# Optimization experiments

Measured on AMD Instinct MI355X. Metric: run time of the kernel, lower is better.

Reference implementation:

```python
import jax, jax.numpy as jnp
import numpy as np

B, NQ, NK = 8, 16384, 16384
FEAT, MID, CTX, OUT = 128, 16, 128, 128
EPS = 1e-5


def setup_inputs() -> dict:
    key = jax.random.key(0)
    ks = jax.random.split(key, 7)
    s_in = 1.0 / np.sqrt(FEAT)
    s_ctx = 1.0 / np.sqrt(CTX)
    return {
        "feature": jax.random.normal(ks[0], (B, NQ, FEAT), dtype=jnp.float32),
        "context": jax.random.normal(ks[1], (B, NK, CTX), dtype=jnp.float32),
        "Wq": jax.random.uniform(ks[2], (FEAT, MID), jnp.float32, -s_in, s_in),
        "Wk": jax.random.uniform(ks[3], (CTX, MID), jnp.float32, -s_ctx, s_ctx),
        "Wv": jax.random.uniform(ks[4], (CTX, OUT), jnp.float32, -s_ctx, s_ctx),
        "gamma": jnp.ones((MID,), jnp.float32),
        "beta": jnp.zeros((MID,), jnp.float32),
    }


def reference(feature, context, Wq, Wk, Wv, gamma, beta):
    # per-token linear projections (QKVTransformV2 with heads=1)
    query = feature @ Wq                     # [B, Nq, mid]
    key = context @ Wk                       # [B, Nk, mid]
    value = context @ Wv                     # [B, Nk, out]
    # softmax over context positions (dim=1)
    sm = jax.nn.softmax(key, axis=1)         # [B, Nk, mid]
    # content lambda: softmax^T @ value -> [B, mid, out]
    lam = jnp.einsum("bnm,bnd->bmd", sm, value)
    # BatchNorm1d(mid) in training mode: stats over (batch, length=out)
    mean = jnp.mean(lam, axis=(0, 2), keepdims=True)
    var = jnp.var(lam, axis=(0, 2), keepdims=True)  # biased, matches torch BN
    bn = (lam - mean) * jax.lax.rsqrt(var + EPS)
    bn = bn * gamma[None, :, None] + beta[None, :, None]
    # final query matmul -> [B, Nq, out]
    return jnp.einsum("bqm,bmd->bqd", query, bn)
```

## Files before the change

kernel.cpp:

```cpp
#include <hip/hip_runtime.h>
#include <cstddef>

#define BATCH 8
#define NQ 16384
#define NK 16384
#define FEAT 128
#define MID 16
#define CTXD 128
#define OUTD 128
#define EPSV 1e-5f

#define OFF_LAM 0
#define OFF_ST  16384
#define OFF_SW  16448
#define OFF_U   16576
#define OFF_S   32960
#define OFF_P   49408
#define NEED_FLOATS (49408 + 8 * 128 * 16 * 128)

__device__ __forceinline__ float readlane_f(float v, int lane) {
    return __uint_as_float(__builtin_amdgcn_readlane(__float_as_uint(v), lane));
}

template <bool PARTIALS>
__global__ __launch_bounds__(256) void k_phase1(
    const float* __restrict__ ctx, const float* __restrict__ Wk,
    float* __restrict__ P, float* __restrict__ S,
    float* __restrict__ U, float* __restrict__ sumwG)
{
    __shared__ float cL[64 * 132];
    __shared__ float wkL[128 * 16];
    const int b    = blockIdx.y;
    const int blk  = blockIdx.x;
    const int t    = threadIdx.x;
    const int lane = t & 63;
    const int g    = __builtin_amdgcn_readfirstlane(t >> 6);

    #pragma unroll
    for (int i = 0; i < 8; ++i) wkL[t + 256 * i] = Wk[t + 256 * i];

    float a00 = 0.f, a01 = 0.f, a10 = 0.f, a11 = 0.f;
    float a20 = 0.f, a21 = 0.f, a30 = 0.f, a31 = 0.f;
    float sw0 = 0.f, sw1 = 0.f, sw2 = 0.f, sw3 = 0.f;
    const size_t rowbase = (size_t)b * NK + (size_t)blk * 128;

    for (int s = 0; s < 2; ++s) {
        __syncthreads();
        {
            const float4* g4 = (const float4*)(ctx + (rowbase + 64 * s) * CTXD);
            float4* c4p = (float4*)cL;
            #pragma unroll
            for (int i = 0; i < 8; ++i) {
                int idx = t + 256 * i;
                c4p[(idx >> 5) * 33 + (idx & 31)] = g4[idx];
            }
        }
        __syncthreads();

        float k0 = 0.f, k1 = 0.f, k2 = 0.f, k3 = 0.f;
        {
            const float4* cr = (const float4*)cL + lane * 33;
            #pragma unroll 8
            for (int kq = 0; kq < 32; ++kq) {
                float4 c4  = cr[kq];
                float4 wr0 = *(const float4*)(wkL + (4 * kq + 0) * 16 + 4 * g);
                float4 wr1 = *(const float4*)(wkL + (4 * kq + 1) * 16 + 4 * g);
                float4 wr2 = *(const float4*)(wkL + (4 * kq + 2) * 16 + 4 * g);
                float4 wr3 = *(const float4*)(wkL + (4 * kq + 3) * 16 + 4 * g);
                k0 += c4.x * wr0.x + c4.y * wr1.x + c4.z * wr2.x + c4.w * wr3.x;
                k1 += c4.x * wr0.y + c4.y * wr1.y + c4.z * wr2.y + c4.w * wr3.y;
                k2 += c4.x * wr0.z + c4.y * wr1.z + c4.z * wr2.z + c4.w * wr3.z;
                k3 += c4.x * wr0.w + c4.y * wr1.w + c4.z * wr2.w + c4.w * wr3.w;
            }
        }
        float w0 = __expf(k0), w1 = __expf(k1), w2 = __expf(k2), w3 = __expf(k3);

        {
            float s0 = w0, s1 = w1, s2 = w2, s3 = w3;
            #pragma unroll
            for (int off = 32; off > 0; off >>= 1) {
                s0 += __shfl_xor(s0, off); s1 += __shfl_xor(s1, off);
                s2 += __shfl_xor(s2, off); s3 += __shfl_xor(s3, off);
            }
            sw0 += s0; sw1 += s1; sw2 += s2; sw3 += s3;
        }

        #pragma unroll 4
        for (int n = 0; n < 64; ++n) {
            float b0 = readlane_f(w0, n);
            float b1 = readlane_f(w1, n);
            float b2 = readlane_f(w2, n);
            float b3 = readlane_f(w3, n);
            float2 c2 = *(const float2*)(cL + n * 132 + 2 * lane);
            a00 += b0 * c2.x; a01 += b0 * c2.y;
            a10 += b1 * c2.x; a11 += b1 * c2.y;
            a20 += b2 * c2.x; a21 += b2 * c2.y;
            a30 += b3 * c2.x; a31 += b3 * c2.y;
        }
    }

    if (PARTIALS) {
        float2* p0 = (float2*)(P + (((size_t)b * 128 + blk) * 16 + 4 * g) * 128 + 2 * lane);
        p0[0]          = make_float2(a00, a01);
        p0[64]         = make_float2(a10, a11);
        p0[128]        = make_float2(a20, a21);
        p0[192]        = make_float2(a30, a31);
        if (lane == 0) {
            S[((size_t)b * 16 + 4 * g + 0) * 128 + blk] = sw0;
            S[((size_t)b * 16 + 4 * g + 1) * 128 + blk] = sw1;
            S[((size_t)b * 16 + 4 * g + 2) * 128 + blk] = sw2;
            S[((size_t)b * 16 + 4 * g + 3) * 128 + blk] = sw3;
        }
    } else {
        float* u0 = U + ((size_t)b * 16 + 4 * g) * 128 + 2 * lane;
        atomicAdd(u0 + 0,   a00); atomicAdd(u0 + 1,   a01);
        atomicAdd(u0 + 128, a10); atomicAdd(u0 + 129, a11);
        atomicAdd(u0 + 256, a20); atomicAdd(u0 + 257, a21);
        atomicAdd(u0 + 384, a30); atomicAdd(u0 + 385, a31);
        if (lane == 0) {
            atomicAdd(&sumwG[b * 16 + 4 * g + 0], sw0);
            atomicAdd(&sumwG[b * 16 + 4 * g + 1], sw1);
            atomicAdd(&sumwG[b * 16 + 4 * g + 2], sw2);
            atomicAdd(&sumwG[b * 16 + 4 * g + 3], sw3);
        }
    }
}

template <bool PARTIALS>
__global__ __launch_bounds__(256) void k_lam(
    const float* __restrict__ P, const float* __restrict__ S,
    const float* __restrict__ U, const float* __restrict__ sumwG,
    const float* __restrict__ Wv, float* __restrict__ lam, float* __restrict__ st)
{
    const int m = blockIdx.x, b = blockIdx.y, t = threadIdx.x;
    __shared__ float uL[128];
    __shared__ float red[256];
    __shared__ float swL;
    const int d = t & 127, h = t >> 7;

    float acc = 0.f;
    if (PARTIALS) {
        const float* p = P + ((size_t)b * 128 * 16 + m) * 128 + d;
        for (int blk = h; blk < 128; blk += 2) acc += p[(size_t)blk * 2048];
    } else {
        if (h == 0) acc = U[((size_t)b * 16 + m) * 128 + d];
    }
    red[t] = acc;

    if (t < 64) {
        float s;
        if (PARTIALS) {
            const float* sp = S + ((size_t)b * 16 + m) * 128;
            s = sp[t] + sp[t + 64];
            #pragma unroll
            for (int off = 32; off > 0; off >>= 1) s += __shfl_xor(s, off);
        } else {
            s = sumwG[b * 16 + m];
        }
        if (t == 0) swL = s;
    }
    __syncthreads();
    if (t < 128) uL[t] = red[t] + red[t + 128];
    __syncthreads();

    float dot = 0.f;
    const float* wv = Wv + h * 64 * OUTD + d;
    #pragma unroll 8
    for (int k = 0; k < 64; ++k) dot += uL[h * 64 + k] * wv[k * OUTD];
    red[t] = dot;
    __syncthreads();
    if (t < 128) {
        float l = (red[t] + red[t + 128]) / swL;
        lam[((size_t)b * 16 + m) * 128 + t] = l;
        float s1 = l, s2 = l * l;
        #pragma unroll
        for (int off = 32; off > 0; off >>= 1) {
            s1 += __shfl_xor(s1, off);
            s2 += __shfl_xor(s2, off);
        }
        if ((t & 63) == 0) {
            atomicAdd(&st[m], s1);
            atomicAdd(&st[16 + m], s2);
        }
    }
}

__global__ __launch_bounds__(256) void k_out(
    const float* __restrict__ feat, const float* __restrict__ Wq,
    const float* __restrict__ lam, const float* __restrict__ st,
    const float* __restrict__ gamma, const float* __restrict__ beta,
    float* __restrict__ out)
{
    __shared__ float fL[64 * 132];
    __shared__ float bnL[16 * 132];
    __shared__ float wqL[128 * 16];
    const int b    = blockIdx.y;
    const int t    = threadIdx.x;
    const int lane = t & 63;
    const size_t r0 = (size_t)blockIdx.x * 64;

    #pragma unroll
    for (int i = 0; i < 8; ++i) wqL[t + 256 * i] = Wq[t + 256 * i];

    #pragma unroll
    for (int i = 0; i < 8; ++i) {
        int e = t + 256 * i;
        int m = e >> 7, d = e & 127;
        float mean = st[m] * (1.f / (BATCH * OUTD));
        float var  = st[16 + m] * (1.f / (BATCH * OUTD)) - mean * mean;
        bnL[m * 132 + d] =
            (lam[((size_t)b * 16 + m) * 128 + d] - mean) * rsqrtf(var + EPSV) * gamma[m] + beta[m];
    }
    {
        const float4* g4 = (const float4*)(feat + ((size_t)b * NQ + r0) * FEAT);
        float4* f4p = (float4*)fL;
        #pragma unroll
        for (int i = 0; i < 8; ++i) {
            int idx = t + 256 * i;
            f4p[(idx >> 5) * 33 + (idx & 31)] = g4[idx];
        }
    }
    __syncthreads();

    float q0 = 0.f, q1 = 0.f, q2 = 0.f, q3 = 0.f;
    {
        const int g = __builtin_amdgcn_readfirstlane(t >> 6);
        const float4* fr = (const float4*)fL + lane * 33;
        #pragma unroll 8
        for (int kq = 0; kq < 32; ++kq) {
            float4 c4  = fr[kq];
            float4 wr0 = *(const float4*)(wqL + (4 * kq + 0) * 16 + 4 * g);
            float4 wr1 = *(const float4*)(wqL + (4 * kq + 1) * 16 + 4 * g);
            float4 wr2 = *(const float4*)(wqL + (4 * kq + 2) * 16 + 4 * g);
            float4 wr3 = *(const float4*)(wqL + (4 * kq + 3) * 16 + 4 * g);
            q0 += c4.x * wr0.x + c4.y * wr1.x + c4.z * wr2.x + c4.w * wr3.x;
            q1 += c4.x * wr0.y + c4.y * wr1.y + c4.z * wr2.y + c4.w * wr3.y;
            q2 += c4.x * wr0.z + c4.y * wr1.z + c4.z * wr2.z + c4.w * wr3.z;
            q3 += c4.x * wr0.w + c4.y * wr1.w + c4.z * wr2.w + c4.w * wr3.w;
        }
    }
    __syncthreads();
    {
        const int g = __builtin_amdgcn_readfirstlane(t >> 6);
        ((float4*)fL)[lane * 5 + g] = make_float4(q0, q1, q2, q3);
    }
    __syncthreads();

    {
        const int nblk = t >> 4;
        const int dq   = t & 15;
        const float4* qL4  = (const float4*)fL;
        const float4* bnL4 = (const float4*)bnL;
        float qv[4][16];
        #pragma unroll
        for (int rr = 0; rr < 4; ++rr) {
            #pragma unroll
            for (int mq = 0; mq < 4; ++mq) {
                float4 v = qL4[(4 * nblk + rr) * 5 + mq];
                qv[rr][4 * mq + 0] = v.x; qv[rr][4 * mq + 1] = v.y;
                qv[rr][4 * mq + 2] = v.z; qv[rr][4 * mq + 3] = v.w;
            }
        }
        float accv[4][8];
        #pragma unroll
        for (int rr = 0; rr < 4; ++rr)
            #pragma unroll
            for (int j = 0; j < 8; ++j) accv[rr][j] = 0.f;

        #pragma unroll
        for (int m = 0; m < 16; ++m) {
            float4 b0 = bnL4[m * 33 + 2 * dq];
            float4 b1 = bnL4[m * 33 + 2 * dq + 1];
            #pragma unroll
            for (int rr = 0; rr < 4; ++rr) {
                float qq = qv[rr][m];
                accv[rr][0] += qq * b0.x; accv[rr][1] += qq * b0.y;
                accv[rr][2] += qq * b0.z; accv[rr][3] += qq * b0.w;
                accv[rr][4] += qq * b1.x; accv[rr][5] += qq * b1.y;
                accv[rr][6] += qq * b1.z; accv[rr][7] += qq * b1.w;
            }
        }
        #pragma unroll
        for (int rr = 0; rr < 4; ++rr) {
            float4* op = (float4*)(out + ((size_t)b * NQ + r0 + 4 * nblk + rr) * OUTD + 8 * dq);
            op[0] = make_float4(accv[rr][0], accv[rr][1], accv[rr][2], accv[rr][3]);
            op[1] = make_float4(accv[rr][4], accv[rr][5], accv[rr][6], accv[rr][7]);
        }
    }
}

extern "C" void kernel_launch(void* const* d_in, const int* in_sizes, int n_in,
                              void* d_out, int out_size, void* d_ws, size_t ws_size,
                              hipStream_t stream)
{
    const float* feat  = (const float*)d_in[0];
    const float* ctx   = (const float*)d_in[1];
    const float* Wq    = (const float*)d_in[2];
    const float* Wk    = (const float*)d_in[3];
    const float* Wv    = (const float*)d_in[4];
    const float* gamma = (const float*)d_in[5];
    const float* beta  = (const float*)d_in[6];
    float* out = (float*)d_out;

    float* ws    = (float*)d_ws;
    float* lam   = ws + OFF_LAM;
    float* st    = ws + OFF_ST;
    float* sumwG = ws + OFF_SW;
    float* U     = ws + OFF_U;
    float* S     = ws + OFF_S;
    float* P     = ws + OFF_P;

    const bool partials = ws_size >= (size_t)NEED_FLOATS * sizeof(float);

    if (partials) {
        hipMemsetAsync((char*)d_ws + OFF_ST * sizeof(float), 0, 64 * sizeof(float), stream);
        k_phase1<true><<<dim3(128, BATCH), 256, 0, stream>>>(ctx, Wk, P, S, U, sumwG);
        k_lam<true><<<dim3(MID, BATCH), 256, 0, stream>>>(P, S, U, sumwG, Wv, lam, st);
    } else {
        hipMemsetAsync((char*)d_ws + OFF_ST * sizeof(float), 0,
                       (OFF_U + 16384 - OFF_ST) * sizeof(float), stream);
        k_phase1<false><<<dim3(128, BATCH), 256, 0, stream>>>(ctx, Wk, P, S, U, sumwG);
        k_lam<false><<<dim3(MID, BATCH), 256, 0, stream>>>(P, S, U, sumwG, Wv, lam, st);
    }
    k_out<<<dim3(NQ / 64, BATCH), 256, 0, stream>>>(feat, Wq, lam, st, gamma, beta, out);
}
```

Baseline: 222.3 us.

## Fold Wq into BN lambda and use bf16 MFMA for key and output matmuls

Precomputes E = Wq @ bn(lambda) per batch as a bf16 128x128 matrix in a new small kernel, so the output kernel becomes one feature @ E matmul done with bf16 MFMA instead of two fp32 FMA stages. The key projection in phase1 also moves to bf16 MFMA, with swizzled LDS layouts and an LDS-staged exp-weight buffer in place of readlane broadcasts. This cuts ALU work in both memory-heavy kernels and adds one extra tiny launch. Rounding inputs to bf16 lowers precision, which affects the softmax exponent and the output.

```diff
diff --git a/kernel.cpp b/kernel.cpp
--- a/kernel.cpp
+++ b/kernel.cpp
@@ -14,12 +14,24 @@
 #define OFF_ST  16384
 #define OFF_SW  16448
 #define OFF_U   16576
-#define OFF_S   32960
-#define OFF_P   49408
-#define NEED_FLOATS (49408 + 8 * 128 * 16 * 128)
-
-__device__ __forceinline__ float readlane_f(float v, int lane) {
-    return __uint_as_float(__builtin_amdgcn_readlane(__float_as_uint(v), lane));
+#define OFF_E   32960
+#define OFF_S   98496
+#define OFF_P   114880
+#define NEED_FLOATS (114880 + 2097152)
+
+typedef __attribute__((ext_vector_type(8))) short bf16x8;
+typedef __attribute__((ext_vector_type(4))) float f32x4;
+
+__device__ __forceinline__ short f2bf(float x) {
+    union { float f; unsigned u; } v; v.f = x;
+    unsigned r = v.u + 0x7fffu + ((v.u >> 16) & 1u);
+    return (short)(r >> 16);
+}
+__device__ __forceinline__ bf16x8 pack8(float4 a, float4 b) {
+    bf16x8 r;
+    r[0] = f2bf(a.x); r[1] = f2bf(a.y); r[2] = f2bf(a.z); r[3] = f2bf(a.w);
+    r[4] = f2bf(b.x); r[5] = f2bf(b.y); r[6] = f2bf(b.z); r[7] = f2bf(b.w);
+    return r;
 }
 
 template <bool PARTIALS>
@@ -28,101 +40,93 @@
     float* __restrict__ P, float* __restrict__ S,
     float* __restrict__ U, float* __restrict__ sumwG)
 {
-    __shared__ float cL[64 * 132];
-    __shared__ float wkL[128 * 16];
-    const int b    = blockIdx.y;
-    const int blk  = blockIdx.x;
-    const int t    = threadIdx.x;
+    __shared__ float cL[64 * 128];
+    __shared__ short wkT[16 * 136];
+    __shared__ float wL[64 * 20];
+    __shared__ float swred[4][16];
+    const int b = blockIdx.y, blk = blockIdx.x, t = threadIdx.x;
     const int lane = t & 63;
-    const int g    = __builtin_amdgcn_readfirstlane(t >> 6);
-
-    #pragma unroll
-    for (int i = 0; i < 8; ++i) wkL[t + 256 * i] = Wk[t + 256 * i];
-
-    float a00 = 0.f, a01 = 0.f, a10 = 0.f, a11 = 0.f;
-    float a20 = 0.f, a21 = 0.f, a30 = 0.f, a31 = 0.f;
-    float sw0 = 0.f, sw1 = 0.f, sw2 = 0.f, sw3 = 0.f;
+    const int wid  = __builtin_amdgcn_readfirstlane(t >> 6);
+    const int rlo = lane & 15, h = lane >> 4;
+
+    #pragma unroll
+    for (int i = 0; i < 8; ++i) {
+        int e = t + 256 * i;
+        wkT[(e & 15) * 136 + (e >> 4)] = f2bf(Wk[e]);
+    }
+
+    float a00=0.f,a01=0.f,a10=0.f,a11=0.f,a20=0.f,a21=0.f,a30=0.f,a31=0.f;
+    float sw = 0.f;
     const size_t rowbase = (size_t)b * NK + (size_t)blk * 128;
 
     for (int s = 0; s < 2; ++s) {
         __syncthreads();
         {
             const float4* g4 = (const float4*)(ctx + (rowbase + 64 * s) * CTXD);
-            float4* c4p = (float4*)cL;
             #pragma unroll
             for (int i = 0; i < 8; ++i) {
                 int idx = t + 256 * i;
-                c4p[(idx >> 5) * 33 + (idx & 31)] = g4[idx];
+                int r = idx >> 5, c = idx & 31;
+                ((float4*)cL)[r * 32 + (c ^ (r & 7))] = g4[idx];
             }
         }
         __syncthreads();
 
-        float k0 = 0.f, k1 = 0.f, k2 = 0.f, k3 = 0.f;
-        {
-            const float4* cr = (const float4*)cL + lane * 33;
-            #pragma unroll 8
-            for (int kq = 0; kq < 32; ++kq) {
-                float4 c4  = cr[kq];
-                float4 wr0 = *(const float4*)(wkL + (4 * kq + 0) * 16 + 4 * g);
-                float4 wr1 = *(const float4*)(wkL + (4 * kq + 1) * 16 + 4 * g);
-                float4 wr2 = *(const float4*)(wkL + (4 * kq + 2) * 16 + 4 * g);
-                float4 wr3 = *(const float4*)(wkL + (4 * kq + 3) * 16 + 4 * g);
-                k0 += c4.x * wr0.x + c4.y * wr1.x + c4.z * wr2.x + c4.w * wr3.x;
-                k1 += c4.x * wr0.y + c4.y * wr1.y + c4.z * wr2.y + c4.w * wr3.y;
-                k2 += c4.x * wr0.z + c4.y * wr1.z + c4.z * wr2.z + c4.w * wr3.z;
-                k3 += c4.x * wr0.w + c4.y * wr1.w + c4.z * wr2.w + c4.w * wr3.w;
-            }
-        }
-        float w0 = __expf(k0), w1 = __expf(k1), w2 = __expf(k2), w3 = __expf(k3);
-
-        {
-            float s0 = w0, s1 = w1, s2 = w2, s3 = w3;
-            #pragma unroll
-            for (int off = 32; off > 0; off >>= 1) {
-                s0 += __shfl_xor(s0, off); s1 += __shfl_xor(s1, off);
-                s2 += __shfl_xor(s2, off); s3 += __shfl_xor(s3, off);
-            }
-            sw0 += s0; sw1 += s1; sw2 += s2; sw3 += s3;
-        }
-
-        #pragma unroll 4
+        const int row = wid * 16 + rlo;
+        f32x4 kacc = {0.f, 0.f, 0.f, 0.f};
+        #pragma unroll
+        for (int ks = 0; ks < 4; ++ks) {
+            float4 A0 = ((const float4*)cL)[row * 32 + ((8*ks + 2*h)     ^ (row & 7))];
+            float4 A1 = ((const float4*)cL)[row * 32 + ((8*ks + 2*h + 1) ^ (row & 7))];
+            bf16x8 af = pack8(A0, A1);
+            bf16x8 bq = *(const bf16x8*)(wkT + rlo * 136 + 32*ks + 8*h);
+            kacc = __builtin_amdgcn_mfma_f32_16x16x32_bf16(af, bq, kacc, 0, 0, 0);
+        }
+        float w0 = __expf(kacc[0]);
+        float w1 = __expf(kacc[1]);
+        float w2 = __expf(kacc[2]);
+        float w3 = __expf(kacc[3]);
+        sw += w0 + w1 + w2 + w3;
+        const int nb = wid * 16 + 4 * h;
+        wL[(nb + 0) * 20 + rlo] = w0;
+        wL[(nb + 1) * 20 + rlo] = w1;
+        wL[(nb + 2) * 20 + rlo] = w2;
+        wL[(nb + 3) * 20 + rlo] = w3;
+        __syncthreads();
+
+        #pragma unroll 8
         for (int n = 0; n < 64; ++n) {
-            float b0 = readlane_f(w0, n);
-            float b1 = readlane_f(w1, n);
-            float b2 = readlane_f(w2, n);
-            float b3 = readlane_f(w3, n);
-            float2 c2 = *(const float2*)(cL + n * 132 + 2 * lane);
-            a00 += b0 * c2.x; a01 += b0 * c2.y;
-            a10 += b1 * c2.x; a11 += b1 * c2.y;
-            a20 += b2 * c2.x; a21 += b2 * c2.y;
-            a30 += b3 * c2.x; a31 += b3 * c2.y;
+            float4 w4 = *(const float4*)(wL + n * 20 + 4 * wid);
+            const float2 c2 = *(const float2*)((const char*)cL + n * 512
+                               + ((((lane >> 1) ^ (n & 7))) << 4) + ((lane & 1) << 3));
+            a00 += w4.x * c2.x; a01 += w4.x * c2.y;
+            a10 += w4.y * c2.x; a11 += w4.y * c2.y;
+            a20 += w4.z * c2.x; a21 += w4.z * c2.y;
+            a30 += w4.w * c2.x; a31 += w4.w * c2.y;
         }
     }
 
     if (PARTIALS) {
-        float2* p0 = (float2*)(P + (((size_t)b * 128 + blk) * 16 + 4 * g) * 128 + 2 * lane);
-        p0[0]          = make_float2(a00, a01);
-        p0[64]         = make_float2(a10, a11);
-        p0[128]        = make_float2(a20, a21);
-        p0[192]        = make_float2(a30, a31);
-        if (lane == 0) {
-            S[((size_t)b * 16 + 4 * g + 0) * 128 + blk] = sw0;
-            S[((size_t)b * 16 + 4 * g + 1) * 128 + blk] = sw1;
-            S[((size_t)b * 16 + 4 * g + 2) * 128 + blk] = sw2;
-            S[((size_t)b * 16 + 4 * g + 3) * 128 + blk] = sw3;
-        }
+        float2* p0 = (float2*)(P + (((size_t)b * 128 + blk) * 16 + 4 * wid) * 128 + 2 * lane);
+        p0[0]   = make_float2(a00, a01);
+        p0[64]  = make_float2(a10, a11);
+        p0[128] = make_float2(a20, a21);
+        p0[192] = make_float2(a30, a31);
     } else {
-        float* u0 = U + ((size_t)b * 16 + 4 * g) * 128 + 2 * lane;
+        float* u0 = U + ((size_t)b * 16 + 4 * wid) * 128 + 2 * lane;
         atomicAdd(u0 + 0,   a00); atomicAdd(u0 + 1,   a01);
         atomicAdd(u0 + 128, a10); atomicAdd(u0 + 129, a11);
         atomicAdd(u0 + 256, a20); atomicAdd(u0 + 257, a21);
         atomicAdd(u0 + 384, a30); atomicAdd(u0 + 385, a31);
-        if (lane == 0) {
-            atomicAdd(&sumwG[b * 16 + 4 * g + 0], sw0);
-            atomicAdd(&sumwG[b * 16 + 4 * g + 1], sw1);
-            atomicAdd(&sumwG[b * 16 + 4 * g + 2], sw2);
-            atomicAdd(&sumwG[b * 16 + 4 * g + 3], sw3);
-        }
+    }
+    sw += __shfl_xor(sw, 16);
+    sw += __shfl_xor(sw, 32);
+    if (lane < 16) swred[wid][lane] = sw;
+    __syncthreads();
+    if (t < 16) {
+        float tot = swred[0][t] + swred[1][t] + swred[2][t] + swred[3][t];
+        if (PARTIALS) S[((size_t)b * 16 + t) * 128 + blk] = tot;
+        else          atomicAdd(&sumwG[b * 16 + t], tot);
     }
 }
 
@@ -185,107 +189,91 @@
     }
 }
 
-__global__ __launch_bounds__(256) void k_out(
-    const float* __restrict__ feat, const float* __restrict__ Wq,
+__global__ __launch_bounds__(256) void k_E(
     const float* __restrict__ lam, const float* __restrict__ st,
-    const float* __restrict__ gamma, const float* __restrict__ beta,
-    float* __restrict__ out)
-{
-    __shared__ float fL[64 * 132];
-    __shared__ float bnL[16 * 132];
-    __shared__ float wqL[128 * 16];
-    const int b    = blockIdx.y;
-    const int t    = threadIdx.x;
-    const int lane = t & 63;
-    const size_t r0 = (size_t)blockIdx.x * 64;
-
-    #pragma unroll
-    for (int i = 0; i < 8; ++i) wqL[t + 256 * i] = Wq[t + 256 * i];
-
+    const float* __restrict__ Wq, const float* __restrict__ gamma,
+    const float* __restrict__ beta, short* __restrict__ Ebuf)
+{
+    const int b = blockIdx.x, t = threadIdx.x;
+    __shared__ float bnL[16 * 128];
+    __shared__ float wqL[128 * 20];
+    #pragma unroll
+    for (int i = 0; i < 8; ++i) {
+        int e = t + 256 * i;
+        wqL[(e >> 4) * 20 + (e & 15)] = Wq[e];
+    }
     #pragma unroll
     for (int i = 0; i < 8; ++i) {
         int e = t + 256 * i;
         int m = e >> 7, d = e & 127;
         float mean = st[m] * (1.f / (BATCH * OUTD));
         float var  = st[16 + m] * (1.f / (BATCH * OUTD)) - mean * mean;
-        bnL[m * 132 + d] =
-            (lam[((size_t)b * 16 + m) * 128 + d] - mean) * rsqrtf(var + EPSV) * gamma[m] + beta[m];
-    }
+        bnL[m * 128 + d] = (lam[((size_t)b * 16 + m) * 128 + d] - mean)
+                           * rsqrtf(var + EPSV) * gamma[m] + beta[m];
+    }
+    __syncthreads();
+    const int k = t & 127, dh = t >> 7;
+    float wq[16];
+    #pragma unroll
+    for (int j = 0; j < 4; ++j) {
+        float4 v = ((const float4*)wqL)[k * 5 + j];
+        wq[4*j] = v.x; wq[4*j+1] = v.y; wq[4*j+2] = v.z; wq[4*j+3] = v.w;
+    }
+    short* eb = Ebuf + (size_t)b * 16384;
+    #pragma unroll 4
+    for (int i = 0; i < 64; ++i) {
+        int d = dh + 2 * i;
+        float s = 0.f;
+        #pragma unroll
+        for (int m = 0; m < 16; ++m) s += wq[m] * bnL[m * 128 + d];
+        eb[d * 128 + k] = f2bf(s);
+    }
+}
+
+__global__ __launch_bounds__(256) void k_out(
+    const float* __restrict__ feat, const short* __restrict__ Ebuf,
+    float* __restrict__ out)
+{
+    __shared__ short eL[128 * 128];
+    const int b = blockIdx.y, t = threadIdx.x;
+    const int lane = t & 63;
+    const int wid  = __builtin_amdgcn_readfirstlane(t >> 6);
+    const int rlo = lane & 15, h = lane >> 4;
+    const size_t r0 = (size_t)blockIdx.x * 64;
+
     {
-        const float4* g4 = (const float4*)(feat + ((size_t)b * NQ + r0) * FEAT);
-        float4* f4p = (float4*)fL;
+        const float4* esrc = (const float4*)(Ebuf + (size_t)b * 16384);
         #pragma unroll
         for (int i = 0; i < 8; ++i) {
             int idx = t + 256 * i;
-            f4p[(idx >> 5) * 33 + (idx & 31)] = g4[idx];
-        }
-    }
-    __syncthreads();
-
-    float q0 = 0.f, q1 = 0.f, q2 = 0.f, q3 = 0.f;
-    {
-        const int g = __builtin_amdgcn_readfirstlane(t >> 6);
-        const float4* fr = (const float4*)fL + lane * 33;
-        #pragma unroll 8
-        for (int kq = 0; kq < 32; ++kq) {
-            float4 c4  = fr[kq];
-            float4 wr0 = *(const float4*)(wqL + (4 * kq + 0) * 16 + 4 * g);
-            float4 wr1 = *(const float4*)(wqL + (4 * kq + 1) * 16 + 4 * g);
-            float4 wr2 = *(const float4*)(wqL + (4 * kq + 2) * 16 + 4 * g);
-            float4 wr3 = *(const float4*)(wqL + (4 * kq + 3) * 16 + 4 * g);
-            q0 += c4.x * wr0.x + c4.y * wr1.x + c4.z * wr2.x + c4.w * wr3.x;
-            q1 += c4.x * wr0.y + c4.y * wr1.y + c4.z * wr2.y + c4.w * wr3.y;
-            q2 += c4.x * wr0.z + c4.y * wr1.z + c4.z * wr2.z + c4.w * wr3.z;
-            q3 += c4.x * wr0.w + c4.y * wr1.w + c4.z * wr2.w + c4.w * wr3.w;
-        }
-    }
-    __syncthreads();
-    {
-        const int g = __builtin_amdgcn_readfirstlane(t >> 6);
-        ((float4*)fL)[lane * 5 + g] = make_float4(q0, q1, q2, q3);
-    }
-    __syncthreads();
-
-    {
-        const int nblk = t >> 4;
-        const int dq   = t & 15;
-        const float4* qL4  = (const float4*)fL;
-        const float4* bnL4 = (const float4*)bnL;
-        float qv[4][16];
-        #pragma unroll
-        for (int rr = 0; rr < 4; ++rr) {
-            #pragma unroll
-            for (int mq = 0; mq < 4; ++mq) {
-                float4 v = qL4[(4 * nblk + rr) * 5 + mq];
-                qv[rr][4 * mq + 0] = v.x; qv[rr][4 * mq + 1] = v.y;
-                qv[rr][4 * mq + 2] = v.z; qv[rr][4 * mq + 3] = v.w;
-            }
-        }
-        float accv[4][8];
-        #pragma unroll
-        for (int rr = 0; rr < 4; ++rr)
-            #pragma unroll
-            for (int j = 0; j < 8; ++j) accv[rr][j] = 0.f;
-
-        #pragma unroll
-        for (int m = 0; m < 16; ++m) {
-            float4 b0 = bnL4[m * 33 + 2 * dq];
-            float4 b1 = bnL4[m * 33 + 2 * dq + 1];
-            #pragma unroll
-            for (int rr = 0; rr < 4; ++rr) {
-                float qq = qv[rr][m];
-                accv[rr][0] += qq * b0.x; accv[rr][1] += qq * b0.y;
-                accv[rr][2] += qq * b0.z; accv[rr][3] += qq * b0.w;
-                accv[rr][4] += qq * b1.x; accv[rr][5] += qq * b1.y;
-                accv[rr][6] += qq * b1.z; accv[rr][7] += qq * b1.w;
-            }
-        }
-        #pragma unroll
-        for (int rr = 0; rr < 4; ++rr) {
-            float4* op = (float4*)(out + ((size_t)b * NQ + r0 + 4 * nblk + rr) * OUTD + 8 * dq);
-            op[0] = make_float4(accv[rr][0], accv[rr][1], accv[rr][2], accv[rr][3]);
-            op[1] = make_float4(accv[rr][4], accv[rr][5], accv[rr][6], accv[rr][7]);
-        }
+            int r = idx >> 4, c = idx & 15;
+            ((float4*)eL)[r * 16 + (c ^ (r & 15))] = esrc[idx];
+        }
+    }
+    __syncthreads();
+
+    const float* fbase = feat + ((size_t)b * NQ + r0 + wid * 16 + rlo) * FEAT + 8 * h;
+    f32x4 acc[8];
+    #pragma unroll
+    for (int ct = 0; ct < 8; ++ct) acc[ct] = (f32x4){0.f, 0.f, 0.f, 0.f};
+
+    #pragma unroll
+    for (int ks = 0; ks < 4; ++ks) {
+        float4 A0 = *(const float4*)(fbase + 32 * ks);
+        float4 A1 = *(const float4*)(fbase + 32 * ks + 4);
+        bf16x8 af = pack8(A0, A1);
+        #pragma unroll
+        for (int ct = 0; ct < 8; ++ct) {
+            bf16x8 bq = *(const bf16x8*)(eL + ((ct * 16 + rlo) * 16 + ((4*ks + h) ^ rlo)) * 8);
+            acc[ct] = __builtin_amdgcn_mfma_f32_16x16x32_bf16(af, bq, acc[ct], 0, 0, 0);
+        }
+    }
+    float* obase = out + ((size_t)b * NQ + r0 + wid * 16 + 4 * h) * OUTD + rlo;
+    #pragma unroll
+    for (int ct = 0; ct < 8; ++ct) {
+        #pragma unroll
+        for (int r = 0; r < 4; ++r)
+            obase[r * OUTD + ct * 16] = acc[ct][r];
     }
 }
 
@@ -307,6 +295,7 @@
     float* st    = ws + OFF_ST;
     float* sumwG = ws + OFF_SW;
     float* U     = ws + OFF_U;
+    short* Ebuf  = (short*)(ws + OFF_E);
     float* S     = ws + OFF_S;
     float* P     = ws + OFF_P;
 
@@ -322,5 +311,6 @@
         k_phase1<false><<<dim3(128, BATCH), 256, 0, stream>>>(ctx, Wk, P, S, U, sumwG);
         k_lam<false><<<dim3(MID, BATCH), 256, 0, stream>>>(P, S, U, sumwG, Wv, lam, st);
     }
-    k_out<<<dim3(NQ / 64, BATCH), 256, 0, stream>>>(feat, Wq, lam, st, gamma, beta, out);
-}
+    k_E<<<dim3(BATCH), 256, 0, stream>>>(lam, st, Wq, gamma, beta, Ebuf);
+    k_out<<<dim3(NQ / 64, BATCH), 256, 0, stream>>>(feat, Ebuf, out);
+}
```

Result: slower. 232.2 us (+4.5%).
